# Kernel optimization log

Measured on AMD Instinct MI355X. Metric: run time of the kernel, lower is better.

Reference implementation:

```python
import jax, jax.numpy as jnp
import numpy as np

B, T = 64, 512
N_EMB, HIDDEN, VOCAB = 768, 256, 3072


def setup_inputs() -> dict:
    key = jax.random.key(0)
    ks = jax.random.split(key, 5)
    def xavier(k, shape):
        bound = float(np.sqrt(6.0 / (shape[0] + shape[1])))
        return jax.random.uniform(k, shape, jnp.float32, -bound, bound)
    return {
        "idx": jax.random.randint(ks[0], (B, T), 0, VOCAB),
        "emb_table": jax.random.normal(ks[1], (VOCAB, N_EMB), jnp.float32),
        "Wxh": xavier(ks[2], (N_EMB, HIDDEN)),
        "Whh": xavier(ks[3], (HIDDEN, HIDDEN)),
        "Wy": xavier(ks[4], (HIDDEN, VOCAB)),
        "By": jnp.zeros((VOCAB,), jnp.float32),
        "Bh": jnp.zeros((HIDDEN,), jnp.float32),
    }


def reference(idx, emb_table, Wxh, Whh, Wy, By, Bh):
    # embedded: [B, T, E] -> scan over time with hidden carry [B, H]
    embedded = emb_table[idx]                      # gather
    xWxh = jnp.einsum('bte,eh->tbh', embedded, Wxh)  # precompute input projection

    def step(hidden, x_t):
        hidden = jnp.tanh(x_t + hidden @ Whh + Bh)
        return hidden, None

    h0 = jnp.zeros((idx.shape[0], Whh.shape[0]), embedded.dtype)
    hidden, _ = jax.lax.scan(step, h0, xWxh)
    # return_sequences=False: only the last step's output is returned
    out = hidden @ Wy + By
    return out, hidden
```

## Files before the change

### kernel.cpp

```cpp
#include <hip/hip_runtime.h>
#include <hip/hip_bf16.h>

typedef _Float16 half8 __attribute__((ext_vector_type(8)));
typedef float f32x4 __attribute__((ext_vector_type(4)));

#define B_SZ 64
#define T_SZ 512
#define E_SZ 768
#define H_SZ 256
#define V_SZ 3072

#define WS_X     0u
#define WS_WT    16777216u
#define WS_WF    17170432u
#define WS_H     17301504u

static __device__ __forceinline__ float fast_tanh(float x) {
  float e = __builtin_amdgcn_exp2f(x * 2.8853900817779268f);
  return 1.0f - 2.0f * __builtin_amdgcn_rcpf(1.0f + e);
}

__global__ __launch_bounds__(256) void k0_convert(
    const float* __restrict__ Wxh,
    const float* __restrict__ Whh,
    _Float16* __restrict__ Wt,
    _Float16* __restrict__ Wf)
{
  int gid = blockIdx.x * 256 + threadIdx.x;
  if (gid < E_SZ * H_SZ) {
    int e = gid >> 8, h = gid & 255;
    Wt[h * E_SZ + e] = (_Float16)Wxh[gid];
  }
  if (gid < 65536) {
    int j = gid & 7, lane = (gid >> 3) & 63, kt = (gid >> 9) & 7, nt = gid >> 12;
    int quad = lane >> 4, n16 = lane & 15;
    int row = kt * 32 + quad * 8 + j, col = nt * 16 + n16;
    Wf[gid] = (_Float16)Whh[row * H_SZ + col];
  }
}

__global__ __launch_bounds__(256) void k1_xproj(
    const int* __restrict__ idx,
    const float* __restrict__ emb,
    const _Float16* __restrict__ Wt,
    _Float16* __restrict__ x)
{
  const int tid  = threadIdx.x;
  const int w    = tid >> 6;
  const int lane = tid & 63;
  const int m16  = lane & 15;
  const int quad = lane >> 4;
  const int r = blockIdx.x * 64 + w * 16 + m16;
  const int t = r >> 6;
  const int b = r & 63;
  const int erow = idx[b * T_SZ + t];
  const float* Arow = emb + (size_t)erow * E_SZ + quad * 8;

  __shared__ __align__(16) _Float16 bp[2][16 * 64 * 8];
  int n_[4], kb_[4];
#pragma unroll
  for (int pp = 0; pp < 4; ++pp) {
    int f = tid + 256 * pp;
    n_[pp]  = ((f >> 6) << 4) | (f & 15);
    kb_[pp] = (f >> 4) & 3;
  }
  uint4 stg[4];
#pragma unroll
  for (int pp = 0; pp < 4; ++pp)
    stg[pp] = *(const uint4*)(Wt + (size_t)n_[pp] * E_SZ + kb_[pp] * 8);
  f32x4 af0 = *(const f32x4*)(Arow);
  f32x4 af1 = *(const f32x4*)(Arow + 4);

  f32x4 acc[16];
#pragma unroll
  for (int n = 0; n < 16; ++n) { f32x4 z = {0.f, 0.f, 0.f, 0.f}; acc[n] = z; }

#pragma unroll
  for (int pp = 0; pp < 4; ++pp)
    *(uint4*)(bp[0] + (size_t)(tid + 256 * pp) * 8) = stg[pp];
  __syncthreads();

#pragma unroll 1
  for (int ki = 0; ki < 24; ++ki) {
    const _Float16* cur = bp[ki & 1];
    f32x4 af0n = af0, af1n = af1;
    if (ki < 23) {
#pragma unroll
      for (int pp = 0; pp < 4; ++pp)
        stg[pp] = *(const uint4*)(Wt + (size_t)n_[pp] * E_SZ + (ki + 1) * 32 + kb_[pp] * 8);
      af0n = *(const f32x4*)(Arow + (ki + 1) * 32);
      af1n = *(const f32x4*)(Arow + (ki + 1) * 32 + 4);
    }
    half8 a;
#pragma unroll
    for (int e = 0; e < 4; ++e) { a[e] = (_Float16)af0[e]; a[4 + e] = (_Float16)af1[e]; }
#pragma unroll
    for (int nt = 0; nt < 16; ++nt) {
      half8 bb = *(const half8*)(cur + (size_t)(nt * 64 + lane) * 8);
      acc[nt] = __builtin_amdgcn_mfma_f32_16x16x32_f16(a, bb, acc[nt], 0, 0, 0);
    }
    if (ki < 23) {
#pragma unroll
      for (int pp = 0; pp < 4; ++pp)
        *(uint4*)(bp[(ki + 1) & 1] + (size_t)(tid + 256 * pp) * 8) = stg[pp];
      __syncthreads();
    }
    af0 = af0n; af1 = af1n;
  }
  const int rbase = blockIdx.x * 64 + w * 16 + quad * 4;
#pragma unroll
  for (int nt = 0; nt < 16; ++nt) {
    const int col = nt * 16 + m16;
#pragma unroll
    for (int rg = 0; rg < 4; ++rg) {
      x[(size_t)(rbase + rg) * H_SZ + col] = (_Float16)acc[nt][rg];
    }
  }
}

#define LDFRAG(C, KT, R0, R1, R2, R3) { \
  uint4 q = Wf4[(((size_t)(w * 4 + C) * 8 + KT) * 64) + lane]; \
  asm volatile("v_accvgpr_write_b32 a" #R0 ", %0" :: "v"(q.x) : "a" #R0); \
  asm volatile("v_accvgpr_write_b32 a" #R1 ", %0" :: "v"(q.y) : "a" #R1); \
  asm volatile("v_accvgpr_write_b32 a" #R2 ", %0" :: "v"(q.z) : "a" #R2); \
  asm volatile("v_accvgpr_write_b32 a" #R3 ", %0" :: "v"(q.w) : "a" #R3); }

#define MFMA_K0(A0, Z) \
  asm volatile( \
    "v_mfma_f32_16x16x32_f16 %[t0], %[a], a[0:3],   %[z]\n\t" \
    "v_mfma_f32_16x16x32_f16 %[t1], %[a], a[32:35], %[z]\n\t" \
    "v_mfma_f32_16x16x32_f16 %[t2], %[a], a[64:67], %[z]\n\t" \
    "v_mfma_f32_16x16x32_f16 %[t3], %[a], a[96:99], %[z]" \
    : [t0] "=&v"(acc0), [t1] "=&v"(acc1), [t2] "=&v"(acc2), [t3] "=&v"(acc3) \
    : [a] "v"(A0), [z] "v"(Z));

#define MFMA_KT(A0, B0, B1, B2, B3) \
  asm volatile( \
    "v_mfma_f32_16x16x32_f16 %[t0], %[a], a[" #B0 "], %[t0]\n\t" \
    "v_mfma_f32_16x16x32_f16 %[t1], %[a], a[" #B1 "], %[t1]\n\t" \
    "v_mfma_f32_16x16x32_f16 %[t2], %[a], a[" #B2 "], %[t2]\n\t" \
    "v_mfma_f32_16x16x32_f16 %[t3], %[a], a[" #B3 "], %[t3]" \
    : [t0] "+v"(acc0), [t1] "+v"(acc1), [t2] "+v"(acc2), [t3] "+v"(acc3) \
    : [a] "v"(A0));

#define MFMA_K7(A0, B0, B1, B2, B3) \
  asm volatile( \
    "v_mfma_f32_16x16x32_f16 %[t0], %[a], a[" #B0 "], %[t0]\n\t" \
    "v_mfma_f32_16x16x32_f16 %[t1], %[a], a[" #B1 "], %[t1]\n\t" \
    "v_mfma_f32_16x16x32_f16 %[t2], %[a], a[" #B2 "], %[t2]\n\t" \
    "v_mfma_f32_16x16x32_f16 %[t3], %[a], a[" #B3 "], %[t3]\n\t" \
    "s_nop 7\n\t" \
    "s_nop 7" \
    : [t0] "+v"(acc0), [t1] "+v"(acc1), [t2] "+v"(acc2), [t3] "+v"(acc3) \
    : [a] "v"(A0));

__global__ __launch_bounds__(256) void k2_rnn(
    const _Float16* __restrict__ Wf,
    const _Float16* __restrict__ x,
    const float* __restrict__ Bh,
    float* __restrict__ hout,
    float* __restrict__ hidout)
{
  const int b    = blockIdx.x;
  const int tid  = threadIdx.x;
  const int w    = tid >> 6;
  const int lane = tid & 63;
  const int quad = lane >> 4;
  __shared__ __align__(16) _Float16 hb[2][H_SZ];
  const uint4* Wf4 = (const uint4*)Wf;

  LDFRAG(0,0,  0,  1,  2,  3)  LDFRAG(0,1,  4,  5,  6,  7)
  LDFRAG(0,2,  8,  9, 10, 11)  LDFRAG(0,3, 12, 13, 14, 15)
  LDFRAG(0,4, 16, 17, 18, 19)  LDFRAG(0,5, 20, 21, 22, 23)
  LDFRAG(0,6, 24, 25, 26, 27)  LDFRAG(0,7, 28, 29, 30, 31)
  LDFRAG(1,0, 32, 33, 34, 35)  LDFRAG(1,1, 36, 37, 38, 39)
  LDFRAG(1,2, 40, 41, 42, 43)  LDFRAG(1,3, 44, 45, 46, 47)
  LDFRAG(1,4, 48, 49, 50, 51)  LDFRAG(1,5, 52, 53, 54, 55)
  LDFRAG(1,6, 56, 57, 58, 59)  LDFRAG(1,7, 60, 61, 62, 63)
  LDFRAG(2,0, 64, 65, 66, 67)  LDFRAG(2,1, 68, 69, 70, 71)
  LDFRAG(2,2, 72, 73, 74, 75)  LDFRAG(2,3, 76, 77, 78, 79)
  LDFRAG(2,4, 80, 81, 82, 83)  LDFRAG(2,5, 84, 85, 86, 87)
  LDFRAG(2,6, 88, 89, 90, 91)  LDFRAG(2,7, 92, 93, 94, 95)
  LDFRAG(3,0, 96, 97, 98, 99)  LDFRAG(3,1,100,101,102,103)
  LDFRAG(3,2,104,105,106,107)  LDFRAG(3,3,108,109,110,111)
  LDFRAG(3,4,112,113,114,115)  LDFRAG(3,5,116,117,118,119)
  LDFRAG(3,6,120,121,122,123)  LDFRAG(3,7,124,125,126,127)

  const float bhj = Bh[tid];
  const _Float16* xp = x + b * H_SZ + tid;
  _Float16 xq = xp[0];
  f32x4 zero4 = {0.f, 0.f, 0.f, 0.f};
  asm volatile("" : "+v"(zero4));
  hb[1][tid] = (_Float16)0.f;
  float hval = 0.f;
  __syncthreads();

#pragma unroll 1
  for (int t = 0; t < T_SZ; ++t) {
    const int tn = (t < T_SZ - 1) ? (t + 1) : t;
    _Float16 xn = xp[(size_t)tn * (B_SZ * H_SZ)];
    const _Float16* hr = hb[(t + 1) & 1];
    half8 va0 = *(const half8*)(hr +   0 + quad * 8);
    half8 va1 = *(const half8*)(hr +  32 + quad * 8);
    half8 va2 = *(const half8*)(hr +  64 + quad * 8);
    half8 va3 = *(const half8*)(hr +  96 + quad * 8);
    half8 va4 = *(const half8*)(hr + 128 + quad * 8);
    half8 va5 = *(const half8*)(hr + 160 + quad * 8);
    half8 va6 = *(const half8*)(hr + 192 + quad * 8);
    half8 va7 = *(const half8*)(hr + 224 + quad * 8);
    f32x4 acc0, acc1, acc2, acc3;
    MFMA_K0(va0, zero4)
    MFMA_KT(va1,   4:7,  36:39,  68:71, 100:103)
    MFMA_KT(va2,  8:11,  40:43,  72:75, 104:107)
    MFMA_KT(va3, 12:15,  44:47,  76:79, 108:111)
    MFMA_KT(va4, 16:19,  48:51,  80:83, 112:115)
    MFMA_KT(va5, 20:23,  52:55,  84:87, 116:119)
    MFMA_KT(va6, 24:27,  56:59,  88:91, 120:123)
    MFMA_K7(va7, 28:31,  60:63,  92:95, 124:127)
    float v0 = acc0[0], v1 = acc1[0], v2 = acc2[0], v3 = acc3[0];
    float ylo = (quad & 1) ? v1 : v0;
    float yhi = (quad & 1) ? v3 : v2;
    float y   = (quad & 2) ? yhi : ylo;
    hval = fast_tanh(y + (float)xq + bhj);
    hb[t & 1][tid] = (_Float16)hval;
    __syncthreads();
    xq = xn;
  }
  hout[b * H_SZ + tid] = hval;
  hidout[b * H_SZ + tid] = hval;
}

__global__ __launch_bounds__(256) void k3_out(
    const float* __restrict__ h,
    const float* __restrict__ Wy,
    const float* __restrict__ By,
    float* __restrict__ out)
{
  __shared__ float hs[H_SZ];
  const int c = blockIdx.x;
  const int b = blockIdx.y;
  const int v = c * 256 + threadIdx.x;
  hs[threadIdx.x] = h[b * H_SZ + threadIdx.x];
  __syncthreads();
  float acc = By[v];
#pragma unroll 8
  for (int jj = 0; jj < H_SZ; ++jj) {
    acc += hs[jj] * Wy[(size_t)jj * V_SZ + v];
  }
  out[(size_t)b * V_SZ + v] = acc;
}

extern "C" void kernel_launch(void* const* d_in, const int* in_sizes, int n_in,
                              void* d_out, int out_size, void* d_ws, size_t ws_size,
                              hipStream_t stream)
{
  const int*   idx = (const int*)d_in[0];
  const float* emb = (const float*)d_in[1];
  const float* Wxh = (const float*)d_in[2];
  const float* Whh = (const float*)d_in[3];
  const float* Wy  = (const float*)d_in[4];
  const float* By  = (const float*)d_in[5];
  const float* Bh  = (const float*)d_in[6];

  char* ws = (char*)d_ws;
  _Float16* x    = (_Float16*)(ws + WS_X);
  _Float16* Wt   = (_Float16*)(ws + WS_WT);
  _Float16* Wf   = (_Float16*)(ws + WS_WF);
  float*    hbuf = (float*)(ws + WS_H);

  float* out    = (float*)d_out;
  float* hidout = out + (size_t)B_SZ * V_SZ;

  k0_convert<<<768, 256, 0, stream>>>(Wxh, Whh, Wt, Wf);
  k1_xproj  <<<512, 256, 0, stream>>>(idx, emb, Wt, x);
  k2_rnn    <<<64, 256, 0, stream>>>(Wf, x, Bh, hbuf, hidout);
  k3_out    <<<dim3(12, 64), 256, 0, stream>>>(hbuf, Wy, By, out);
}
```

Baseline: 386.3 us.

## Process two batch rows per RNN block to interleave recurrent MFMA chains

Each k2_rnn workgroup now advances two batch rows at once, halving the grid from 64 to 32 blocks. The two independent MFMA dependency chains run back to back, so one row's MFMA latency can hide behind the other's, and the per-step barrier cost is shared by two rows. In exchange each step does twice the serial work per block, and half as many CUs are used.

```diff
diff --git a/kernel.cpp b/kernel.cpp
--- a/kernel.cpp
+++ b/kernel.cpp
@@ -125,25 +125,25 @@
   asm volatile("v_accvgpr_write_b32 a" #R2 ", %0" :: "v"(q.z) : "a" #R2); \
   asm volatile("v_accvgpr_write_b32 a" #R3 ", %0" :: "v"(q.w) : "a" #R3); }
 
-#define MFMA_K0(A0, Z) \
+#define MFMA_K0(A0, Z, C0, C1, C2, C3) \
   asm volatile( \
     "v_mfma_f32_16x16x32_f16 %[t0], %[a], a[0:3],   %[z]\n\t" \
     "v_mfma_f32_16x16x32_f16 %[t1], %[a], a[32:35], %[z]\n\t" \
     "v_mfma_f32_16x16x32_f16 %[t2], %[a], a[64:67], %[z]\n\t" \
     "v_mfma_f32_16x16x32_f16 %[t3], %[a], a[96:99], %[z]" \
-    : [t0] "=&v"(acc0), [t1] "=&v"(acc1), [t2] "=&v"(acc2), [t3] "=&v"(acc3) \
+    : [t0] "=&v"(C0), [t1] "=&v"(C1), [t2] "=&v"(C2), [t3] "=&v"(C3) \
     : [a] "v"(A0), [z] "v"(Z));
 
-#define MFMA_KT(A0, B0, B1, B2, B3) \
+#define MFMA_KT(A0, B0, B1, B2, B3, C0, C1, C2, C3) \
   asm volatile( \
     "v_mfma_f32_16x16x32_f16 %[t0], %[a], a[" #B0 "], %[t0]\n\t" \
     "v_mfma_f32_16x16x32_f16 %[t1], %[a], a[" #B1 "], %[t1]\n\t" \
     "v_mfma_f32_16x16x32_f16 %[t2], %[a], a[" #B2 "], %[t2]\n\t" \
     "v_mfma_f32_16x16x32_f16 %[t3], %[a], a[" #B3 "], %[t3]" \
-    : [t0] "+v"(acc0), [t1] "+v"(acc1), [t2] "+v"(acc2), [t3] "+v"(acc3) \
+    : [t0] "+v"(C0), [t1] "+v"(C1), [t2] "+v"(C2), [t3] "+v"(C3) \
     : [a] "v"(A0));
 
-#define MFMA_K7(A0, B0, B1, B2, B3) \
+#define MFMA_K7(A0, B0, B1, B2, B3, C0, C1, C2, C3) \
   asm volatile( \
     "v_mfma_f32_16x16x32_f16 %[t0], %[a], a[" #B0 "], %[t0]\n\t" \
     "v_mfma_f32_16x16x32_f16 %[t1], %[a], a[" #B1 "], %[t1]\n\t" \
@@ -151,8 +151,18 @@
     "v_mfma_f32_16x16x32_f16 %[t3], %[a], a[" #B3 "], %[t3]\n\t" \
     "s_nop 7\n\t" \
     "s_nop 7" \
-    : [t0] "+v"(acc0), [t1] "+v"(acc1), [t2] "+v"(acc2), [t3] "+v"(acc3) \
+    : [t0] "+v"(C0), [t1] "+v"(C1), [t2] "+v"(C2), [t3] "+v"(C3) \
     : [a] "v"(A0));
+
+#define MFMA_GROUP(V0,V1,V2,V3,V4,V5,V6,V7, C0,C1,C2,C3, Z) \
+  MFMA_K0(V0, Z, C0,C1,C2,C3) \
+  MFMA_KT(V1,   4:7,  36:39,  68:71, 100:103, C0,C1,C2,C3) \
+  MFMA_KT(V2,  8:11,  40:43,  72:75, 104:107, C0,C1,C2,C3) \
+  MFMA_KT(V3, 12:15,  44:47,  76:79, 108:111, C0,C1,C2,C3) \
+  MFMA_KT(V4, 16:19,  48:51,  80:83, 112:115, C0,C1,C2,C3) \
+  MFMA_KT(V5, 20:23,  52:55,  84:87, 116:119, C0,C1,C2,C3) \
+  MFMA_KT(V6, 24:27,  56:59,  88:91, 120:123, C0,C1,C2,C3) \
+  MFMA_K7(V7, 28:31,  60:63,  92:95, 124:127, C0,C1,C2,C3)
 
 __global__ __launch_bounds__(256) void k2_rnn(
     const _Float16* __restrict__ Wf,
@@ -161,12 +171,13 @@
     float* __restrict__ hout,
     float* __restrict__ hidout)
 {
-  const int b    = blockIdx.x;
+  const int b0   = blockIdx.x * 2;
+  const int b1   = b0 + 1;
   const int tid  = threadIdx.x;
   const int w    = tid >> 6;
   const int lane = tid & 63;
   const int quad = lane >> 4;
-  __shared__ __align__(16) _Float16 hb[2][H_SZ];
+  __shared__ __align__(16) _Float16 hb[2][2][H_SZ];
   const uint4* Wf4 = (const uint4*)Wf;
 
   LDFRAG(0,0,  0,  1,  2,  3)  LDFRAG(0,1,  4,  5,  6,  7)
@@ -187,47 +198,65 @@
   LDFRAG(3,6,120,121,122,123)  LDFRAG(3,7,124,125,126,127)
 
   const float bhj = Bh[tid];
-  const _Float16* xp = x + b * H_SZ + tid;
-  _Float16 xq = xp[0];
+  const _Float16* xp0 = x + b0 * H_SZ + tid;
+  const _Float16* xp1 = x + b1 * H_SZ + tid;
+  _Float16 xq0 = xp0[0], xq1 = xp1[0];
   f32x4 zero4 = {0.f, 0.f, 0.f, 0.f};
   asm volatile("" : "+v"(zero4));
-  hb[1][tid] = (_Float16)0.f;
-  float hval = 0.f;
+  hb[1][0][tid] = (_Float16)0.f;
+  hb[1][1][tid] = (_Float16)0.f;
+  float h0 = 0.f, h1 = 0.f;
   __syncthreads();
 
 #pragma unroll 1
   for (int t = 0; t < T_SZ; ++t) {
     const int tn = (t < T_SZ - 1) ? (t + 1) : t;
-    _Float16 xn = xp[(size_t)tn * (B_SZ * H_SZ)];
-    const _Float16* hr = hb[(t + 1) & 1];
-    half8 va0 = *(const half8*)(hr +   0 + quad * 8);
-    half8 va1 = *(const half8*)(hr +  32 + quad * 8);
-    half8 va2 = *(const half8*)(hr +  64 + quad * 8);
-    half8 va3 = *(const half8*)(hr +  96 + quad * 8);
-    half8 va4 = *(const half8*)(hr + 128 + quad * 8);
-    half8 va5 = *(const half8*)(hr + 160 + quad * 8);
-    half8 va6 = *(const half8*)(hr + 192 + quad * 8);
-    half8 va7 = *(const half8*)(hr + 224 + quad * 8);
-    f32x4 acc0, acc1, acc2, acc3;
-    MFMA_K0(va0, zero4)
-    MFMA_KT(va1,   4:7,  36:39,  68:71, 100:103)
-    MFMA_KT(va2,  8:11,  40:43,  72:75, 104:107)
-    MFMA_KT(va3, 12:15,  44:47,  76:79, 108:111)
-    MFMA_KT(va4, 16:19,  48:51,  80:83, 112:115)
-    MFMA_KT(va5, 20:23,  52:55,  84:87, 116:119)
-    MFMA_KT(va6, 24:27,  56:59,  88:91, 120:123)
-    MFMA_K7(va7, 28:31,  60:63,  92:95, 124:127)
-    float v0 = acc0[0], v1 = acc1[0], v2 = acc2[0], v3 = acc3[0];
-    float ylo = (quad & 1) ? v1 : v0;
-    float yhi = (quad & 1) ? v3 : v2;
-    float y   = (quad & 2) ? yhi : ylo;
-    hval = fast_tanh(y + (float)xq + bhj);
-    hb[t & 1][tid] = (_Float16)hval;
+    _Float16 xn0 = xp0[(size_t)tn * (B_SZ * H_SZ)];
+    _Float16 xn1 = xp1[(size_t)tn * (B_SZ * H_SZ)];
+    const _Float16* hr0 = hb[(t + 1) & 1][0];
+    const _Float16* hr1 = hb[(t + 1) & 1][1];
+    half8 va0 = *(const half8*)(hr0 +   0 + quad * 8);
+    half8 va1 = *(const half8*)(hr0 +  32 + quad * 8);
+    half8 va2 = *(const half8*)(hr0 +  64 + quad * 8);
+    half8 va3 = *(const half8*)(hr0 +  96 + quad * 8);
+    half8 va4 = *(const half8*)(hr0 + 128 + quad * 8);
+    half8 va5 = *(const half8*)(hr0 + 160 + quad * 8);
+    half8 va6 = *(const half8*)(hr0 + 192 + quad * 8);
+    half8 va7 = *(const half8*)(hr0 + 224 + quad * 8);
+    half8 vb0 = *(const half8*)(hr1 +   0 + quad * 8);
+    half8 vb1 = *(const half8*)(hr1 +  32 + quad * 8);
+    half8 vb2 = *(const half8*)(hr1 +  64 + quad * 8);
+    half8 vb3 = *(const half8*)(hr1 +  96 + quad * 8);
+    half8 vb4 = *(const half8*)(hr1 + 128 + quad * 8);
+    half8 vb5 = *(const half8*)(hr1 + 160 + quad * 8);
+    half8 vb6 = *(const half8*)(hr1 + 192 + quad * 8);
+    half8 vb7 = *(const half8*)(hr1 + 224 + quad * 8);
+    f32x4 ac0, ac1, ac2, ac3, bc0, bc1, bc2, bc3;
+    MFMA_GROUP(va0,va1,va2,va3,va4,va5,va6,va7, ac0,ac1,ac2,ac3, zero4)
+    MFMA_GROUP(vb0,vb1,vb2,vb3,vb4,vb5,vb6,vb7, bc0,bc1,bc2,bc3, zero4)
+    {
+      float v0 = ac0[0], v1 = ac1[0], v2 = ac2[0], v3 = ac3[0];
+      float ylo = (quad & 1) ? v1 : v0;
+      float yhi = (quad & 1) ? v3 : v2;
+      float y   = (quad & 2) ? yhi : ylo;
+      h0 = fast_tanh(y + (float)xq0 + bhj);
+      hb[t & 1][0][tid] = (_Float16)h0;
+    }
+    {
+      float v0 = bc0[0], v1 = bc1[0], v2 = bc2[0], v3 = bc3[0];
+      float ylo = (quad & 1) ? v1 : v0;
+      float yhi = (quad & 1) ? v3 : v2;
+      float y   = (quad & 2) ? yhi : ylo;
+      h1 = fast_tanh(y + (float)xq1 + bhj);
+      hb[t & 1][1][tid] = (_Float16)h1;
+    }
     __syncthreads();
-    xq = xn;
-  }
-  hout[b * H_SZ + tid] = hval;
-  hidout[b * H_SZ + tid] = hval;
+    xq0 = xn0; xq1 = xn1;
+  }
+  hout[b0 * H_SZ + tid] = h0;
+  hout[b1 * H_SZ + tid] = h1;
+  hidout[b0 * H_SZ + tid] = h0;
+  hidout[b1 * H_SZ + tid] = h1;
 }
 
 __global__ __launch_bounds__(256) void k3_out(
@@ -273,6 +302,6 @@
 
   k0_convert<<<768, 256, 0, stream>>>(Wxh, Whh, Wt, Wf);
   k1_xproj  <<<512, 256, 0, stream>>>(idx, emb, Wt, x);
-  k2_rnn    <<<64, 256, 0, stream>>>(Wf, x, Bh, hbuf, hidout);
+  k2_rnn    <<<32, 256, 0, stream>>>(Wf, x, Bh, hbuf, hidout);
   k3_out    <<<dim3(12, 64), 256, 0, stream>>>(hbuf, Wy, By, out);
 }
```

Result: slower. 530.9 us (+37.4%).

## Split RNN recurrence across 8 waves with two output tiles per wave

Applied to the files above, without the earlier changes.

The per-sequence recurrence kernel now runs with 512 threads (8 waves) instead of 256. Each wave holds two 16-column tiles of Whh in AGPRs instead of four, which halves the serial MFMA chain per timestep. Only quad 0 writes the new hidden state to shared memory. This shortens each step's critical path at the cost of a wider block barrier per step and redundant tanh work in the other quads.

```diff
diff --git a/kernel.cpp b/kernel.cpp
--- a/kernel.cpp
+++ b/kernel.cpp
@@ -119,7 +119,7 @@
 }
 
 #define LDFRAG(C, KT, R0, R1, R2, R3) { \
-  uint4 q = Wf4[(((size_t)(w * 4 + C) * 8 + KT) * 64) + lane]; \
+  uint4 q = Wf4[(((size_t)(w * 2 + C) * 8 + KT) * 64) + lane]; \
   asm volatile("v_accvgpr_write_b32 a" #R0 ", %0" :: "v"(q.x) : "a" #R0); \
   asm volatile("v_accvgpr_write_b32 a" #R1 ", %0" :: "v"(q.y) : "a" #R1); \
   asm volatile("v_accvgpr_write_b32 a" #R2 ", %0" :: "v"(q.z) : "a" #R2); \
@@ -128,33 +128,27 @@
 #define MFMA_K0(A0, Z) \
   asm volatile( \
     "v_mfma_f32_16x16x32_f16 %[t0], %[a], a[0:3],   %[z]\n\t" \
-    "v_mfma_f32_16x16x32_f16 %[t1], %[a], a[32:35], %[z]\n\t" \
-    "v_mfma_f32_16x16x32_f16 %[t2], %[a], a[64:67], %[z]\n\t" \
-    "v_mfma_f32_16x16x32_f16 %[t3], %[a], a[96:99], %[z]" \
-    : [t0] "=&v"(acc0), [t1] "=&v"(acc1), [t2] "=&v"(acc2), [t3] "=&v"(acc3) \
+    "v_mfma_f32_16x16x32_f16 %[t1], %[a], a[32:35], %[z]" \
+    : [t0] "=&v"(acc0), [t1] "=&v"(acc1) \
     : [a] "v"(A0), [z] "v"(Z));
 
-#define MFMA_KT(A0, B0, B1, B2, B3) \
+#define MFMA_KT(A0, B0, B1) \
+  asm volatile( \
+    "v_mfma_f32_16x16x32_f16 %[t0], %[a], a[" #B0 "], %[t0]\n\t" \
+    "v_mfma_f32_16x16x32_f16 %[t1], %[a], a[" #B1 "], %[t1]" \
+    : [t0] "+v"(acc0), [t1] "+v"(acc1) \
+    : [a] "v"(A0));
+
+#define MFMA_K7(A0, B0, B1) \
   asm volatile( \
     "v_mfma_f32_16x16x32_f16 %[t0], %[a], a[" #B0 "], %[t0]\n\t" \
     "v_mfma_f32_16x16x32_f16 %[t1], %[a], a[" #B1 "], %[t1]\n\t" \
-    "v_mfma_f32_16x16x32_f16 %[t2], %[a], a[" #B2 "], %[t2]\n\t" \
-    "v_mfma_f32_16x16x32_f16 %[t3], %[a], a[" #B3 "], %[t3]" \
-    : [t0] "+v"(acc0), [t1] "+v"(acc1), [t2] "+v"(acc2), [t3] "+v"(acc3) \
-    : [a] "v"(A0));
-
-#define MFMA_K7(A0, B0, B1, B2, B3) \
-  asm volatile( \
-    "v_mfma_f32_16x16x32_f16 %[t0], %[a], a[" #B0 "], %[t0]\n\t" \
-    "v_mfma_f32_16x16x32_f16 %[t1], %[a], a[" #B1 "], %[t1]\n\t" \
-    "v_mfma_f32_16x16x32_f16 %[t2], %[a], a[" #B2 "], %[t2]\n\t" \
-    "v_mfma_f32_16x16x32_f16 %[t3], %[a], a[" #B3 "], %[t3]\n\t" \
     "s_nop 7\n\t" \
     "s_nop 7" \
-    : [t0] "+v"(acc0), [t1] "+v"(acc1), [t2] "+v"(acc2), [t3] "+v"(acc3) \
+    : [t0] "+v"(acc0), [t1] "+v"(acc1) \
     : [a] "v"(A0));
 
-__global__ __launch_bounds__(256) void k2_rnn(
+__global__ __launch_bounds__(512) void k2_rnn(
     const _Float16* __restrict__ Wf,
     const _Float16* __restrict__ x,
     const float* __restrict__ Bh,
@@ -166,6 +160,7 @@
   const int w    = tid >> 6;
   const int lane = tid & 63;
   const int quad = lane >> 4;
+  const int n16  = lane & 15;
   __shared__ __align__(16) _Float16 hb[2][H_SZ];
   const uint4* Wf4 = (const uint4*)Wf;
 
@@ -177,28 +172,25 @@
   LDFRAG(1,2, 40, 41, 42, 43)  LDFRAG(1,3, 44, 45, 46, 47)
   LDFRAG(1,4, 48, 49, 50, 51)  LDFRAG(1,5, 52, 53, 54, 55)
   LDFRAG(1,6, 56, 57, 58, 59)  LDFRAG(1,7, 60, 61, 62, 63)
-  LDFRAG(2,0, 64, 65, 66, 67)  LDFRAG(2,1, 68, 69, 70, 71)
-  LDFRAG(2,2, 72, 73, 74, 75)  LDFRAG(2,3, 76, 77, 78, 79)
-  LDFRAG(2,4, 80, 81, 82, 83)  LDFRAG(2,5, 84, 85, 86, 87)
-  LDFRAG(2,6, 88, 89, 90, 91)  LDFRAG(2,7, 92, 93, 94, 95)
-  LDFRAG(3,0, 96, 97, 98, 99)  LDFRAG(3,1,100,101,102,103)
-  LDFRAG(3,2,104,105,106,107)  LDFRAG(3,3,108,109,110,111)
-  LDFRAG(3,4,112,113,114,115)  LDFRAG(3,5,116,117,118,119)
-  LDFRAG(3,6,120,121,122,123)  LDFRAG(3,7,124,125,126,127)
-
-  const float bhj = Bh[tid];
-  const _Float16* xp = x + b * H_SZ + tid;
-  _Float16 xq = xp[0];
+
+  const int col0 = w * 32 + n16;
+  const int col1 = col0 + 16;
+  const float bh0 = Bh[col0];
+  const float bh1 = Bh[col1];
+  const _Float16* xp0 = x + b * H_SZ + col0;
+  const _Float16* xp1 = x + b * H_SZ + col1;
+  _Float16 xq0 = xp0[0], xq1 = xp1[0];
   f32x4 zero4 = {0.f, 0.f, 0.f, 0.f};
   asm volatile("" : "+v"(zero4));
-  hb[1][tid] = (_Float16)0.f;
-  float hval = 0.f;
+  if (tid < H_SZ) hb[1][tid] = (_Float16)0.f;
+  float h0 = 0.f, h1 = 0.f;
   __syncthreads();
 
 #pragma unroll 1
   for (int t = 0; t < T_SZ; ++t) {
     const int tn = (t < T_SZ - 1) ? (t + 1) : t;
-    _Float16 xn = xp[(size_t)tn * (B_SZ * H_SZ)];
+    _Float16 xn0 = xp0[(size_t)tn * (B_SZ * H_SZ)];
+    _Float16 xn1 = xp1[(size_t)tn * (B_SZ * H_SZ)];
     const _Float16* hr = hb[(t + 1) & 1];
     half8 va0 = *(const half8*)(hr +   0 + quad * 8);
     half8 va1 = *(const half8*)(hr +  32 + quad * 8);
@@ -208,26 +200,28 @@
     half8 va5 = *(const half8*)(hr + 160 + quad * 8);
     half8 va6 = *(const half8*)(hr + 192 + quad * 8);
     half8 va7 = *(const half8*)(hr + 224 + quad * 8);
-    f32x4 acc0, acc1, acc2, acc3;
+    f32x4 acc0, acc1;
     MFMA_K0(va0, zero4)
-    MFMA_KT(va1,   4:7,  36:39,  68:71, 100:103)
-    MFMA_KT(va2,  8:11,  40:43,  72:75, 104:107)
-    MFMA_KT(va3, 12:15,  44:47,  76:79, 108:111)
-    MFMA_KT(va4, 16:19,  48:51,  80:83, 112:115)
-    MFMA_KT(va5, 20:23,  52:55,  84:87, 116:119)
-    MFMA_KT(va6, 24:27,  56:59,  88:91, 120:123)
-    MFMA_K7(va7, 28:31,  60:63,  92:95, 124:127)
-    float v0 = acc0[0], v1 = acc1[0], v2 = acc2[0], v3 = acc3[0];
-    float ylo = (quad & 1) ? v1 : v0;
-    float yhi = (quad & 1) ? v3 : v2;
-    float y   = (quad & 2) ? yhi : ylo;
-    hval = fast_tanh(y + (float)xq + bhj);
-    hb[t & 1][tid] = (_Float16)hval;
+    MFMA_KT(va1,  4:7,  36:39)
+    MFMA_KT(va2,  8:11, 40:43)
+    MFMA_KT(va3, 12:15, 44:47)
+    MFMA_KT(va4, 16:19, 48:51)
+    MFMA_KT(va5, 20:23, 52:55)
+    MFMA_KT(va6, 24:27, 56:59)
+    MFMA_K7(va7, 28:31, 60:63)
+    h0 = fast_tanh(acc0[0] + (float)xq0 + bh0);
+    h1 = fast_tanh(acc1[0] + (float)xq1 + bh1);
+    if (quad == 0) {
+      hb[t & 1][col0] = (_Float16)h0;
+      hb[t & 1][col1] = (_Float16)h1;
+    }
     __syncthreads();
-    xq = xn;
-  }
-  hout[b * H_SZ + tid] = hval;
-  hidout[b * H_SZ + tid] = hval;
+    xq0 = xn0; xq1 = xn1;
+  }
+  if (quad == 0) {
+    hout[b * H_SZ + col0] = h0;  hout[b * H_SZ + col1] = h1;
+    hidout[b * H_SZ + col0] = h0; hidout[b * H_SZ + col1] = h1;
+  }
 }
 
 __global__ __launch_bounds__(256) void k3_out(
@@ -273,6 +267,6 @@
 
   k0_convert<<<768, 256, 0, stream>>>(Wxh, Whh, Wt, Wf);
   k1_xproj  <<<512, 256, 0, stream>>>(idx, emb, Wt, x);
-  k2_rnn    <<<64, 256, 0, stream>>>(Wf, x, Bh, hbuf, hidout);
+  k2_rnn    <<<64, 512, 0, stream>>>(Wf, x, Bh, hbuf, hidout);
   k3_out    <<<dim3(12, 64), 256, 0, stream>>>(hbuf, Wy, By, out);
 }
```

After: 387.6 us. Within noise of the previous version (+0.3%).
